# Performance work log

Measured on AMD Instinct MI355X. Metric: run time of the kernel, lower is better.

The kernel has to match this reference:

```python
import math
import jax, jax.numpy as jnp
from jax import lax
import numpy as np

SCORE_THR = 0.5
IOU_THR = 0.7
MIN_SIZE = 1.0
BBOX_CLIP = math.log(1000.0 / 16.0)

FEAT_SIZES = [100, 50, 25, 13, 7]
STRIDES = [8, 16, 32, 64, 128]
RATIOS = (0.5, 1.0, 2.0)
C = 256
A = 3
N = 2


def _make_priors(fs, stride):
    base = stride * 4.0
    ys, xs = np.meshgrid(np.arange(fs), np.arange(fs), indexing='ij')
    cx = (xs + 0.5) * stride
    cy = (ys + 0.5) * stride
    pri = []
    for r in RATIOS:
        w = base / np.sqrt(r)
        h = base * np.sqrt(r)
        pri.append(np.stack([cx - w / 2, cy - h / 2, cx + w / 2, cy + h / 2], axis=-1))
    pri = np.stack(pri, axis=2)  # (fs, fs, A, 4): H,W,A order matches permute/reshape
    return jnp.asarray(pri.reshape(-1, 4), dtype=jnp.float32)


def setup_inputs():
    key = jax.random.key(0)
    ks = jax.random.split(key, 8)
    inp = {}
    for i, fs in enumerate(FEAT_SIZES):
        inp[f'fmap{i}'] = jax.random.normal(jax.random.fold_in(ks[0], i), (N, C, fs, fs), dtype=jnp.float32)
        inp[f'priors{i}'] = _make_priors(fs, STRIDES[i])
    sc = 0.02
    inp['conv_w'] = jax.random.normal(ks[1], (C, C, 3, 3), jnp.float32) * sc
    inp['conv_b'] = jnp.zeros((C,), jnp.float32)
    inp['log_w'] = jax.random.normal(ks[2], (A, C, 1, 1), jnp.float32) * sc
    inp['log_b'] = jnp.zeros((A,), jnp.float32)
    inp['reg_w'] = jax.random.normal(ks[3], (A * 4, C, 1, 1), jnp.float32) * sc
    inp['reg_b'] = jnp.zeros((A * 4,), jnp.float32)
    inp['imsizes'] = jnp.full((N, 2), 800, dtype=jnp.int32)  # (h, w) per image
    inp['lvtop'] = 500
    inp['imtop'] = 100
    return inp


def _conv(x, w, b, pad):
    y = lax.conv_general_dilated(x, w, (1, 1), pad, dimension_numbers=('NCHW', 'OIHW', 'NCHW'))
    return y + b[None, :, None, None]


def _decode(reg, pri):
    pw = pri[..., 2] - pri[..., 0]
    ph = pri[..., 3] - pri[..., 1]
    pcx = pri[..., 0] + 0.5 * pw
    pcy = pri[..., 1] + 0.5 * ph
    dx, dy = reg[..., 0], reg[..., 1]
    dw = jnp.minimum(reg[..., 2], BBOX_CLIP)
    dh = jnp.minimum(reg[..., 3], BBOX_CLIP)
    cx = dx * pw + pcx
    cy = dy * ph + pcy
    w = jnp.exp(dw) * pw
    h = jnp.exp(dh) * ph
    return jnp.stack([cx - 0.5 * w, cy - 0.5 * h, cx + 0.5 * w, cy + 0.5 * h], axis=-1)


def _head(x, priors, conv_w, conv_b, log_w, log_b, reg_w, reg_b, lvtop):
    n = x.shape[0]
    h = jax.nn.relu(_conv(x, conv_w, conv_b, 'SAME'))
    reg = _conv(h, reg_w, reg_b, 'VALID').transpose(0, 2, 3, 1).reshape(n, -1, 4)
    log = _conv(h, log_w, log_b, 'VALID').transpose(0, 2, 3, 1).reshape(n, -1)
    k = min(lvtop, log.shape[1])
    vals, top = lax.top_k(log, k)                           # (n, k)
    reg = jnp.take_along_axis(reg, top[..., None], axis=1)  # (n, k, 4)
    pri = priors[top]                                       # (n, k, 4)
    return _decode(reg, pri), vals, k


def _box_iou(a, b):
    area_a = (a[:, 2] - a[:, 0]) * (a[:, 3] - a[:, 1])
    area_b = (b[:, 2] - b[:, 0]) * (b[:, 3] - b[:, 1])
    lt = jnp.maximum(a[:, None, :2], b[None, :, :2])
    rb = jnp.minimum(a[:, None, 2:], b[None, :, 2:])
    wh = jnp.clip(rb - lt, 0.0)
    inter = wh[..., 0] * wh[..., 1]
    return inter / (area_a[:, None] + area_b[None, :] - inter + 1e-9)


def _forward(fmaps, priors, conv_w, conv_b, log_w, log_b, reg_w, reg_b, imsizes, lvtop, imtop):
    tups = [_head(x, p, conv_w, conv_b, log_w, log_b, reg_w, reg_b, lvtop)
            for x, p in zip(fmaps, priors)]
    boxes = jnp.concatenate([t[0] for t in tups], axis=1)                 # (n, D, 4)
    obj = jax.nn.sigmoid(jnp.concatenate([t[1] for t in tups], axis=1))   # (n, D)
    lvlen = jnp.asarray([t[2] for t in tups])
    n, D = obj.shape
    boxes = boxes.reshape(-1, 4)
    obj = obj.reshape(-1)
    K = n * D
    imidx = jnp.arange(K) // D
    valid = obj >= SCORE_THR                                # score filter (masked, not nonzero)
    hw = imsizes[imidx].astype(jnp.float32)                 # (K, 2) = (h, w)
    x1 = jnp.clip(boxes[:, 0], 0.0, hw[:, 1])
    y1 = jnp.clip(boxes[:, 1], 0.0, hw[:, 0])
    x2 = jnp.clip(boxes[:, 2], 0.0, hw[:, 1])
    y2 = jnp.clip(boxes[:, 3], 0.0, hw[:, 0])
    boxes = jnp.stack([x1, y1, x2, y2], axis=-1)
    valid &= (x2 - x1 >= MIN_SIZE) & (y2 - y1 >= MIN_SIZE)  # remove_small
    lvidx = jnp.searchsorted(jnp.cumsum(lvlen), jnp.arange(K) % D, side='right')
    groups = imidx * 10 + lvidx
    scores = jnp.where(valid, obj, -jnp.inf)
    order = jnp.argsort(-scores)                            # global score order; groups gate suppression
    b, g, v, ii = boxes[order], groups[order], valid[order], imidx[order]
    iou = _box_iou(b, b)                                    # (K, K)
    ar = jnp.arange(K)
    def body(i, keep):
        sup = (iou[i] > IOU_THR) & (g == g[i]) & (ar > i)
        return jnp.where(keep[i], keep & ~sup, keep)
    keep = lax.fori_loop(0, K, body, v)                     # greedy batched NMS
    def select(i):
        m = keep & (ii == i)
        sel = jnp.argsort(~m)[:imtop]                       # stable: kept boxes in score order
        val = m[sel]
        bx = jnp.where(val[:, None], b[sel], 0.0)
        ix = jnp.where(val, i, -1)
        return bx, ix
    bx, ix = jax.vmap(select)(jnp.arange(n))
    return bx.reshape(n * imtop, 4), ix.reshape(n * imtop)


def reference(fmap0, fmap1, fmap2, fmap3, fmap4, priors0, priors1, priors2, priors3, priors4,
              conv_w, conv_b, log_w, log_b, reg_w, reg_b, imsizes, lvtop, imtop):
    return _forward([fmap0, fmap1, fmap2, fmap3, fmap4],
                    [priors0, priors1, priors2, priors3, priors4],
                    conv_w, conv_b, log_w, log_b, reg_w, reg_b, imsizes, lvtop, imtop)
```

## Files before the change

### kernel.cpp

```cpp
#include <hip/hip_runtime.h>
#include <math.h>


#define N_IMG 2
#define C_CH  256
#define D_PER 2147
#define K_TOT 4294
#define CONV_BLOCKS 1912
#define CPX 239

typedef double v4d __attribute__((ext_vector_type(4)));

__constant__ int c_Ml[5]     = {30000, 7500, 1875, 507, 147};
__constant__ int c_kl[5]     = {500, 500, 500, 500, 147};
__constant__ int c_logoff[5] = {0, 60000, 75000, 78750, 79764};
__constant__ int c_regoff[5] = {0, 240000, 300000, 315000, 319056};
__constant__ int c_fs[5]     = {100, 50, 25, 13, 7};
__constant__ int c_npt[5]    = {13, 7, 4, 2, 1};
__constant__ int c_E[5]      = {10000, 2500, 625, 169, 49};
__constant__ int c_cumbl[6]  = {0, 1352, 1744, 1872, 1904, 1912};
__constant__ int c_hcum[6]   = {0, 157, 197, 207, 210, 211};
__constant__ size_t c_hoff[5] = {0, 5120000, 6400000, 6720000, 6806528};

__global__ void transpose_w_kernel(const float* __restrict__ w,
                                   double* __restrict__ wT2) {
  int i = blockIdx.x * 256 + threadIdx.x;
  if (i >= 589824) return;
  int q = i % 2304;
  int slab = i / 2304;
  int cobi = slab >> 6, ch = slab & 63;
  int tap = q / 256;
  int rem = q % 256;
  int ci = rem >> 6, co = rem & 63;
  wT2[i] =
      (double)w[(size_t)(cobi * 64 + co) * 2304 + (ch * 4 + ci) * 9 + tap];
}

template <typename T>
__global__ __launch_bounds__(256) void conv_fused_kernel(
    const float* __restrict__ x0, const float* __restrict__ x1,
    const float* __restrict__ x2, const float* __restrict__ x3,
    const float* __restrict__ x4, const double* __restrict__ wT2,
    const float* __restrict__ bias, T* __restrict__ h) {
  __shared__ __align__(16) double s_in[4 * 120];
  __shared__ __align__(16) double s_w[2304];
  int tid = threadIdx.x;
  int bid = (blockIdx.x & 7) * CPX + (blockIdx.x >> 3);
  int l = 0;
  while (bid >= c_cumbl[l + 1]) ++l;
  int r = bid - c_cumbl[l];
  int fs = c_fs[l], npt = c_npt[l];
  int tiles = npt * npt;
  int tile = r % tiles;
  int cn = r / tiles;
  int cobi = cn & 3, n = cn >> 2;
  int ptx = tile % npt, pty = tile / npt;
  int px0 = ptx * 8, py0 = pty * 8;
  int E = fs * fs;
  const float* xl;
  switch (l) {
    case 0: xl = x0; break;
    case 1: xl = x1; break;
    case 2: xl = x2; break;
    case 3: xl = x3; break;
    default: xl = x4; break;
  }
  const float* xn = xl + (size_t)n * C_CH * E;
  T* hl = h + c_hoff[l];

  int lane = tid & 63;
  int wv = tid >> 6;
  int lx = lane & 15;
  int lk = lane >> 4;

  double ind0 = (lk == 0) ? 1.0 : 0.0;
  v4d pr1 = __builtin_amdgcn_mfma_f64_16x16x4f64((double)lx, ind0,
                                                 (v4d)0.0, 0, 0, 0);
  v4d pr2 = __builtin_amdgcn_mfma_f64_16x16x4f64(ind0, (double)lx,
                                                 (v4d)0.0, 0, 0, 0);
  int coL[4], pxL[4];
#pragma unroll
  for (int q = 0; q < 4; ++q) {
    coL[q] = (int)pr1[q];
    pxL[q] = (int)pr2[q];
  }

  int in_dst[2], in_src[2];
#pragma unroll
  for (int it = 0; it < 2; ++it) {
    int idx = tid + it * 256;
    in_dst[it] = -1;
    in_src[it] = -1;
    if (idx < 400) {
      int ci = idx / 100, rr2 = idx % 100;
      int hy = rr2 / 10, hx = rr2 % 10;
      int gy = py0 - 1 + hy, gx = px0 - 1 + hx;
      in_dst[it] = ci * 120 + hy * 12 + hx;
      if (gy >= 0 && gy < fs && gx >= 0 && gx < fs)
        in_src[it] = ci * E + gy * fs + gx;
    }
  }

  const double* aBase = s_w + lk * 64 + wv * 16 + lx;
  const double* bBase[4];
#pragma unroll
  for (int p = 0; p < 4; ++p) {
    int pxidx = p * 16 + lx;
    bBase[p] = s_in + lk * 120 + (pxidx >> 3) * 12 + (pxidx & 7);
  }

  v4d acc[4];
#pragma unroll
  for (int p = 0; p < 4; ++p) acc[p] = (v4d)0.0;

  const double2* wsrc0 = (const double2*)(wT2 + (size_t)cobi * 64 * 2304);

  for (int ch = 0; ch < 64; ++ch) {
    const float* xc = xn + (size_t)ch * 4 * E;
#pragma unroll
    for (int it = 0; it < 2; ++it) {
      if (in_dst[it] >= 0)
        s_in[in_dst[it]] = (in_src[it] >= 0) ? (double)xc[in_src[it]] : 0.0;
    }
    {
      const double2* src = wsrc0 + (size_t)ch * 1152;
      double2* dst = (double2*)s_w;
#pragma unroll
      for (int k = 0; k < 5; k++) {
        int idx = tid + k * 256;
        if (idx < 1152) dst[idx] = src[idx];
      }
    }
    __syncthreads();
#pragma unroll
    for (int ky = 0; ky < 3; ++ky) {
#pragma unroll
      for (int kx = 0; kx < 3; ++kx) {
        int tap = ky * 3 + kx;
        double av = aBase[tap * 256];
        int boff = ky * 12 + kx;
#pragma unroll
        for (int p = 0; p < 4; ++p) {
          double bv = bBase[p][boff];
          acc[p] = __builtin_amdgcn_mfma_f64_16x16x4f64(av, bv, acc[p],
                                                        0, 0, 0);
        }
      }
    }
    __syncthreads();
  }

#pragma unroll
  for (int p = 0; p < 4; ++p) {
#pragma unroll
    for (int rr2 = 0; rr2 < 4; ++rr2) {
      int pxidx = p * 16 + pxL[rr2];
      int gy = py0 + (pxidx >> 3), gx = px0 + (pxidx & 7);
      int co = cobi * 64 + wv * 16 + coL[rr2];
      if (gy < fs && gx < fs) {
        double v = acc[p][rr2] + (double)bias[co];
        hl[((size_t)n * C_CH + co) * E + gy * fs + gx] = (T)fmax(v, 0.0);
      }
    }
  }
}

template <typename T>
__global__ __launch_bounds__(256) void heads_fused_kernel(
    const T* __restrict__ h, const float* __restrict__ logw,
    const float* __restrict__ logb, const float* __restrict__ regw,
    const float* __restrict__ regb, double* __restrict__ logits,
    double* __restrict__ regs) {
  __shared__ float s_wh[256][16];
  __shared__ double s_red[4][15][64];
  int tid = threadIdx.x;
  int n = blockIdx.y;
  int cidx = blockIdx.x;
  int l = 0;
  while (cidx >= c_hcum[l + 1]) ++l;
  int chunk = cidx - c_hcum[l];
  int E = c_E[l];
  int px0 = chunk * 64;
  const T* hl = h + c_hoff[l];
  double* logits_l = logits + c_logoff[l];
  double* regs_l = regs + c_regoff[l];

  for (int idx = tid; idx < 4096; idx += 256) {
    int c = idx >> 4, j = idx & 15;
    float v = 0.f;
    if (j < 3) v = logw[j * 256 + c];
    else if (j < 15) v = regw[(j - 3) * 256 + c];
    s_wh[c][j] = v;
  }
  __syncthreads();

  int p = tid & 63, c4 = tid >> 6;
  int pix = px0 + p;
  bool act = pix < E;
  double acc[15];
#pragma unroll
  for (int j = 0; j < 15; j++) acc[j] = 0.0;
  if (act) {
    const T* hp = hl + ((size_t)n * C_CH + c4 * 64) * E + pix;
    for (int cc = 0; cc < 64; ++cc) {
      double hv = (double)hp[(size_t)cc * E];
      const float* wr = &s_wh[c4 * 64 + cc][0];
#pragma unroll
      for (int j = 0; j < 15; j++)
        acc[j] = fma((double)wr[j], hv, acc[j]);
    }
  }
#pragma unroll
  for (int j = 0; j < 15; j++) s_red[c4][j][p] = acc[j];
  __syncthreads();
  if (act) {
    int M = E * 3;
    for (int j = c4; j < 15; j += 4) {
      double v = s_red[0][j][p] + s_red[1][j][p] + s_red[2][j][p] +
                 s_red[3][j][p];
      if (j < 3) {
        logits_l[(size_t)n * M + pix * 3 + j] = v + (double)logb[j];
      } else {
        int rj = j - 3, a = rj >> 2, coord = rj & 3;
        regs_l[((size_t)n * M + pix * 3 + a) * 4 + coord] =
            v + (double)regb[rj];
      }
    }
  }
}

__device__ __forceinline__ unsigned long long d2key(double v) {
  unsigned long long ub = (unsigned long long)__double_as_longlong(v);
  return (ub >> 63) ? ~ub : (ub | 0x8000000000000000ull);
}

#define TK_CH 30
union TkShared {
  struct {
    int histw[16][256];
    int hist[256];
    int sgt[1024];
    int seq[1024];
  } a;
  struct {
    unsigned long long u[512];
    int idx[512];
    int keep[512];
    int ps[512];
    int m;
    double bx[512][4];
    unsigned long long mask[512][8];
  } b;
};

__global__ __launch_bounds__(1024) void topk_nms_kernel(
    const double* __restrict__ logits, const double* __restrict__ regs,
    const float* __restrict__ p0, const float* __restrict__ p1,
    const float* __restrict__ p2, const float* __restrict__ p3,
    const float* __restrict__ p4, const int* __restrict__ imsizes,
    double* __restrict__ g_box, unsigned long long* __restrict__ g_u,
    int* __restrict__ g_cnt) {
  __shared__ TkShared sh;
  __shared__ int s_sel[512];
  __shared__ unsigned long long s_prefix;
  __shared__ int s_r;
  int bid = blockIdx.x;
  int n = bid / 5, l = bid % 5;
  int M = c_Ml[l], k = c_kl[l];
  const double* lg = logits + c_logoff[l] + (size_t)n * M;
  int tid = threadIdx.x;
  if (tid == 0) { s_prefix = 0ull; s_r = k; }

  int chunk = (M + 1023) >> 10;
  int i0 = tid * chunk, i1 = min(M, i0 + chunk);
  int cnt = i1 - i0;
  if (cnt < 0) cnt = 0;
  unsigned long long kv[TK_CH];
#pragma unroll
  for (int q = 0; q < TK_CH; q++)
    if (q < cnt) kv[q] = d2key(lg[i0 + q]);
  int wid = tid >> 6;
  __syncthreads();

  for (int pass = 0; pass < 8; ++pass) {
    int shift = 56 - pass * 8;
    for (int i = tid; i < 4096; i += 1024) ((int*)sh.a.histw)[i] = 0;
    __syncthreads();
    unsigned long long pfx = s_prefix;
    int rr = s_r;
#pragma unroll
    for (int q = 0; q < TK_CH; q++) {
      if (q < cnt) {
        unsigned long long u = kv[q];
        if (pass == 0 || (u >> (shift + 8)) == pfx)
          atomicAdd(&sh.a.histw[wid][(int)((u >> shift) & 255ull)], 1);
      }
    }
    __syncthreads();
    if (tid < 256) {
      int s = 0;
#pragma unroll
      for (int w = 0; w < 16; w++) s += sh.a.histw[w][tid];
      sh.a.hist[tid] = s;
    }
    __syncthreads();
    if (tid == 0) {
      int s = 0, beta = 0;
      for (int b = 255; b >= 0; --b) {
        if (s + sh.a.hist[b] >= rr) { beta = b; break; }
        s += sh.a.hist[b];
      }
      s_prefix = (pfx << 8) | (unsigned long long)beta;
      s_r = rr - s;
    }
    __syncthreads();
  }
  unsigned long long T = s_prefix;
  int need = s_r;
  int cgt = 0, ceq = 0;
#pragma unroll
  for (int q = 0; q < TK_CH; q++) {
    if (q < cnt) {
      cgt += (kv[q] > T);
      ceq += (kv[q] == T);
    }
  }
  sh.a.sgt[tid] = cgt;
  sh.a.seq[tid] = ceq;
  __syncthreads();
  for (int o = 1; o < 1024; o <<= 1) {
    int a = (tid >= o) ? sh.a.sgt[tid - o] : 0;
    int b2 = (tid >= o) ? sh.a.seq[tid - o] : 0;
    __syncthreads();
    sh.a.sgt[tid] += a;
    sh.a.seq[tid] += b2;
    __syncthreads();
  }
  int gt_total = sh.a.sgt[1023];
  int pg = sh.a.sgt[tid] - cgt, pe = sh.a.seq[tid] - ceq;
#pragma unroll
  for (int q = 0; q < TK_CH; q++) {
    if (q < cnt) {
      unsigned long long u = kv[q];
      if (u > T) {
        s_sel[pg++] = i0 + q;
      } else if (u == T) {
        if (pe < need) s_sel[gt_total + pe] = i0 + q;
        pe++;
      }
    }
  }
  __syncthreads();

  const float* pp;
  switch (l) {
    case 0: pp = p0; break;
    case 1: pp = p1; break;
    case 2: pp = p2; break;
    case 3: pp = p3; break;
    default: pp = p4; break;
  }
  const double* regs_l = regs + c_regoff[l];
  double imh = (double)imsizes[n * 2 + 0], imw = (double)imsizes[n * 2 + 1];
  const double BCLIP = 4.1351665567423560;
  if (tid < 512) {
    unsigned long long key = 0ull;
    sh.b.idx[tid] = tid;
    sh.b.keep[tid] = 0;
    if (tid < k) {
      int aidx = s_sel[tid];
      double lv = lg[aidx];
      double obj = 1.0 / (1.0 + exp(-lv));
      const double* rp = regs_l + ((size_t)n * M + aidx) * 4;
      const float* pr = pp + (size_t)aidx * 4;
      double px1 = pr[0], py1 = pr[1], px2 = pr[2], py2 = pr[3];
      double pw = px2 - px1, ph = py2 - py1;
      double pcx = px1 + 0.5 * pw, pcy = py1 + 0.5 * ph;
      double dx = rp[0], dy = rp[1];
      double dw = fmin(rp[2], BCLIP), dh = fmin(rp[3], BCLIP);
      double cx = dx * pw + pcx, cy = dy * ph + pcy;
      double w = exp(dw) * pw, hh = exp(dh) * ph;
      double x1 = cx - 0.5 * w, y1 = cy - 0.5 * hh;
      double x2 = cx + 0.5 * w, y2 = cy + 0.5 * hh;
      x1 = fmin(fmax(x1, 0.0), imw);
      x2 = fmin(fmax(x2, 0.0), imw);
      y1 = fmin(fmax(y1, 0.0), imh);
      y2 = fmin(fmax(y2, 0.0), imh);
      bool valid = (obj >= 0.5) && ((x2 - x1) >= 1.0) && ((y2 - y1) >= 1.0);
      sh.b.bx[tid][0] = x1;
      sh.b.bx[tid][1] = y1;
      sh.b.bx[tid][2] = x2;
      sh.b.bx[tid][3] = y2;
      if (valid) key = d2key(obj);
    }
    sh.b.u[tid] = key;
  }
  if (tid == 0) sh.b.m = 0;
  __syncthreads();

  for (int kk = 2; kk <= 512; kk <<= 1) {
    for (int j = kk >> 1; j > 0; j >>= 1) {
      if (tid < 512) {
        int i = tid, ixj = i ^ j;
        if (ixj > i) {
          unsigned long long ua = sh.b.u[i], ub = sh.b.u[ixj];
          int ia = sh.b.idx[i], ib = sh.b.idx[ixj];
          bool up = ((i & kk) == 0);
          bool aAfterB = (ua < ub) || (ua == ub && ia > ib);
          bool sw = up ? aAfterB : !aAfterB && (ua != ub || ia != ib);
          if (sw) {
            sh.b.u[i] = ub; sh.b.u[ixj] = ua;
            sh.b.idx[i] = ib; sh.b.idx[ixj] = ia;
          }
        }
      }
      __syncthreads();
    }
  }
  if (tid < 512) {
    if (sh.b.u[tid] != 0ull && (tid == 511 || sh.b.u[tid + 1] == 0ull))
      sh.b.m = tid + 1;
  }
  __syncthreads();
  int m = sh.b.m;

  if (tid < 512 && tid < m) {
    int i = tid;
    const double* A = sh.b.bx[sh.b.idx[i]];
    double ax1 = A[0], ay1 = A[1], ax2 = A[2], ay2 = A[3];
    double areaA = (ax2 - ax1) * (ay2 - ay1);
    unsigned long long row[8] = {0, 0, 0, 0, 0, 0, 0, 0};
    for (int j = i + 1; j < m; ++j) {
      const double* B = sh.b.bx[sh.b.idx[j]];
      double bx1 = B[0], by1 = B[1], bx2 = B[2], by2 = B[3];
      double areaB = (bx2 - bx1) * (by2 - by1);
      double lx = fmax(ax1, bx1), ly = fmax(ay1, by1);
      double rx = fmin(ax2, bx2), ry = fmin(ay2, by2);
      double iw = fmax(rx - lx, 0.0), ih = fmax(ry - ly, 0.0);
      double inter = iw * ih;
      double iou = inter / (areaA + areaB - inter + 1e-9);
      if (iou > 0.7) row[j >> 6] |= (1ull << (j & 63));
    }
#pragma unroll
    for (int w2 = 0; w2 < 8; ++w2) sh.b.mask[i][w2] = row[w2];
  }
  __syncthreads();

  if (tid == 0) {
    unsigned long long remv[8] = {0, 0, 0, 0, 0, 0, 0, 0};
    for (int i = 0; i < m; ++i) {
      if (!((remv[i >> 6] >> (i & 63)) & 1ull)) {
        sh.b.keep[i] = 1;
#pragma unroll
        for (int w2 = 0; w2 < 8; ++w2) remv[w2] |= sh.b.mask[i][w2];
      }
    }
  }
  __syncthreads();

  if (tid < 512) sh.b.ps[tid] = sh.b.keep[tid];
  __syncthreads();
  for (int o = 1; o < 512; o <<= 1) {
    int v = 0;
    if (tid < 512 && tid >= o) v = sh.b.ps[tid - o];
    __syncthreads();
    if (tid < 512) sh.b.ps[tid] += v;
    __syncthreads();
  }
  if (tid < 512 && sh.b.keep[tid]) {
    int pos = sh.b.ps[tid] - 1;
    const double* B = sh.b.bx[sh.b.idx[tid]];
    size_t gbase = (size_t)bid * 512 + pos;
#pragma unroll
    for (int q = 0; q < 4; q++) g_box[gbase * 4 + q] = B[q];
    g_u[gbase] = sh.b.u[tid];
  }
  if (tid == 0) g_cnt[bid] = (m > 0) ? sh.b.ps[511] : 0;
}

__global__ __launch_bounds__(256) void select_kernel(
    const double* __restrict__ g_box, const unsigned long long* __restrict__ g_u,
    const int* __restrict__ g_cnt, float* __restrict__ out) {
  __shared__ unsigned long long s_u[5][512];
  __shared__ int s_pick[100];
  __shared__ int s_total;
  int n = blockIdx.x;
  int tid = threadIdx.x;
  int cnts[5];
#pragma unroll
  for (int l = 0; l < 5; l++) cnts[l] = g_cnt[n * 5 + l];
  for (int idx = tid; idx < 5 * 512; idx += 256) {
    int l = idx >> 9, r = idx & 511;
    s_u[l][r] = (r < cnts[l]) ? g_u[(size_t)(n * 5 + l) * 512 + r] : 0ull;
  }
  __syncthreads();
  if (tid == 0) {
    int hd[5] = {0, 0, 0, 0, 0};
    int t = 0;
    while (t < 100) {
      int bl = -1;
      unsigned long long bu = 0ull;
      for (int l = 0; l < 5; l++) {
        if (hd[l] < cnts[l] && s_u[l][hd[l]] > bu) {
          bu = s_u[l][hd[l]];
          bl = l;
        }
      }
      if (bl < 0) break;
      s_pick[t++] = bl * 512 + hd[bl];
      hd[bl]++;
    }
    s_total = t;
  }
  __syncthreads();
  int total = s_total;
  for (int t = tid; t < 100; t += 256) {
    if (t < total) {
      int pk = s_pick[t];
      int l = pk >> 9, r = pk & 511;
      size_t gbase = (size_t)(n * 5 + l) * 512 + r;
#pragma unroll
      for (int q = 0; q < 4; q++)
        out[(n * 100 + t) * 4 + q] = (float)g_box[gbase * 4 + q];
      out[800 + n * 100 + t] = (float)n;
    } else {
#pragma unroll
      for (int q = 0; q < 4; q++) out[(n * 100 + t) * 4 + q] = 0.0f;
      out[800 + n * 100 + t] = -1.0f;
    }
  }
}

extern "C" void kernel_launch(void* const* d_in, const int* in_sizes, int n_in,
                              void* d_out, int out_size, void* d_ws,
                              size_t ws_size, hipStream_t stream) {
  (void)in_sizes; (void)n_in; (void)out_size;
  const float* fmap[5];
  const float* priors[5];
  for (int l = 0; l < 5; l++) {
    fmap[l] = (const float*)d_in[2 * l];
    priors[l] = (const float*)d_in[2 * l + 1];
  }
  const float* conv_w = (const float*)d_in[10];
  const float* conv_b = (const float*)d_in[11];
  const float* log_w = (const float*)d_in[12];
  const float* log_b = (const float*)d_in[13];
  const float* reg_w = (const float*)d_in[14];
  const float* reg_b = (const float*)d_in[15];
  const int* imsizes = (const int*)d_in[16];
  float* out = (float*)d_out;

  bool f64h = ws_size >= (size_t)66000000;

  char* base = (char*)d_ws;
  size_t off = 0;
  auto alloc = [&](size_t bytes) -> void* {
    off = (off + 255) & ~(size_t)255;
    void* p = base + off;
    off += bytes;
    return p;
  };
  double* wT2 = (double*)alloc(589824ull * 8);
  void* hraw = alloc(6831616ull * (f64h ? 8 : 4));
  double* logits = (double*)alloc(80058ull * 8);
  double* regs = (double*)alloc(320232ull * 8);
  double* g_box = (double*)alloc(10ull * 512 * 4 * 8);
  unsigned long long* g_u = (unsigned long long*)alloc(10ull * 512 * 8);
  int* g_cnt = (int*)alloc(10 * 4);

  transpose_w_kernel<<<2304, 256, 0, stream>>>(conv_w, wT2);

  if (f64h) {
    conv_fused_kernel<double><<<CONV_BLOCKS, 256, 0, stream>>>(
        fmap[0], fmap[1], fmap[2], fmap[3], fmap[4], wT2, conv_b,
        (double*)hraw);
    heads_fused_kernel<double><<<dim3(211, 2), 256, 0, stream>>>(
        (double*)hraw, log_w, log_b, reg_w, reg_b, logits, regs);
  } else {
    conv_fused_kernel<float><<<CONV_BLOCKS, 256, 0, stream>>>(
        fmap[0], fmap[1], fmap[2], fmap[3], fmap[4], wT2, conv_b,
        (float*)hraw);
    heads_fused_kernel<float><<<dim3(211, 2), 256, 0, stream>>>(
        (float*)hraw, log_w, log_b, reg_w, reg_b, logits, regs);
  }
  topk_nms_kernel<<<10, 1024, 0, stream>>>(
      logits, regs, priors[0], priors[1], priors[2], priors[3], priors[4],
      imsizes, g_box, g_u, g_cnt);
  select_kernel<<<2, 256, 0, stream>>>(g_box, g_u, g_cnt, out);
}
```

Measured before the change: 1.076 ms.

## Load conv weights directly into registers and double-buffer input tiles

The conv kernel no longer stages weights in shared memory. Each thread loads its 9 per-tap weight values straight from global memory into registers, and the next channel's weights and inputs are prefetched while the current channel's MFMAs run. The input tile uses a two-slot shared buffer, so only one barrier per channel is needed instead of two. This trades higher register pressure and redundant global weight reads across lanes for less LDS traffic and fewer synchronizations.

```diff
diff --git a/kernel.cpp b/kernel.cpp
--- a/kernel.cpp
+++ b/kernel.cpp
@@ -42,8 +42,7 @@
     const float* __restrict__ x2, const float* __restrict__ x3,
     const float* __restrict__ x4, const double* __restrict__ wT2,
     const float* __restrict__ bias, T* __restrict__ h) {
-  __shared__ __align__(16) double s_in[4 * 120];
-  __shared__ __align__(16) double s_w[2304];
+  __shared__ __align__(16) double s_in[2 * 480];
   int tid = threadIdx.x;
   int bid = (blockIdx.x & 7) * CPX + (blockIdx.x >> 3);
   int l = 0;
@@ -101,53 +100,74 @@
     }
   }
 
-  const double* aBase = s_w + lk * 64 + wv * 16 + lx;
-  const double* bBase[4];
+  int bOff[4];
 #pragma unroll
   for (int p = 0; p < 4; ++p) {
     int pxidx = p * 16 + lx;
-    bBase[p] = s_in + lk * 120 + (pxidx >> 3) * 12 + (pxidx & 7);
+    bOff[p] = lk * 120 + (pxidx >> 3) * 12 + (pxidx & 7);
   }
 
   v4d acc[4];
 #pragma unroll
   for (int p = 0; p < 4; ++p) acc[p] = (v4d)0.0;
 
-  const double2* wsrc0 = (const double2*)(wT2 + (size_t)cobi * 64 * 2304);
+  const double* wptr =
+      wT2 + (size_t)cobi * 64 * 2304 + lk * 64 + wv * 16 + lx;
+
+  double wcur[9], wnxt[9];
+#pragma unroll
+  for (int t = 0; t < 9; ++t) wcur[t] = wptr[t * 256];
+  {
+    float v0[2];
+#pragma unroll
+    for (int it = 0; it < 2; ++it)
+      v0[it] = (in_dst[it] >= 0 && in_src[it] >= 0) ? xn[in_src[it]] : 0.f;
+#pragma unroll
+    for (int it = 0; it < 2; ++it)
+      if (in_dst[it] >= 0) s_in[in_dst[it]] = (double)v0[it];
+  }
+  __syncthreads();
 
   for (int ch = 0; ch < 64; ++ch) {
-    const float* xc = xn + (size_t)ch * 4 * E;
-#pragma unroll
-    for (int it = 0; it < 2; ++it) {
-      if (in_dst[it] >= 0)
-        s_in[in_dst[it]] = (in_src[it] >= 0) ? (double)xc[in_src[it]] : 0.0;
-    }
-    {
-      const double2* src = wsrc0 + (size_t)ch * 1152;
-      double2* dst = (double2*)s_w;
-#pragma unroll
-      for (int k = 0; k < 5; k++) {
-        int idx = tid + k * 256;
-        if (idx < 1152) dst[idx] = src[idx];
-      }
-    }
-    __syncthreads();
+    int buf = ch & 1;
+    bool more = (ch + 1 < 64);
+    float inx[2];
+    if (more) {
+      const float* xc1 = xn + (size_t)(ch + 1) * 4 * E;
+#pragma unroll
+      for (int it = 0; it < 2; ++it)
+        inx[it] =
+            (in_dst[it] >= 0 && in_src[it] >= 0) ? xc1[in_src[it]] : 0.f;
+      const double* wn = wptr + 2304;
+#pragma unroll
+      for (int t = 0; t < 9; ++t) wnxt[t] = wn[t * 256];
+    }
+    const double* bb = s_in + buf * 480;
 #pragma unroll
     for (int ky = 0; ky < 3; ++ky) {
 #pragma unroll
       for (int kx = 0; kx < 3; ++kx) {
         int tap = ky * 3 + kx;
-        double av = aBase[tap * 256];
+        double av = wcur[tap];
         int boff = ky * 12 + kx;
 #pragma unroll
         for (int p = 0; p < 4; ++p) {
-          double bv = bBase[p][boff];
+          double bv = bb[bOff[p] + boff];
           acc[p] = __builtin_amdgcn_mfma_f64_16x16x4f64(av, bv, acc[p],
                                                         0, 0, 0);
         }
       }
     }
-    __syncthreads();
+    if (more) {
+      double* db = s_in + (buf ^ 1) * 480;
+#pragma unroll
+      for (int it = 0; it < 2; ++it)
+        if (in_dst[it] >= 0) db[in_dst[it]] = (double)inx[it];
+#pragma unroll
+      for (int t = 0; t < 9; ++t) wcur[t] = wnxt[t];
+    }
+    __syncthreads();
+    wptr += 2304;
   }
 
 #pragma unroll
```

Result: faster. 1.035 ms (-3.8%).
